# Kernel tuning notes

Hardware: AMD Instinct MI355X
Metric: run time of the kernel (lower is better)

The kernel has to match this reference:

```python
import jax, jax.numpy as jnp
import numpy as np

POOL = (2, 2)
STRIDES = (2, 2)


def _extract_patches(x, ph, pw, sh, sw):
    # x: [B, W, H, C] -> [B, Wo, Ho, ph*pw, C], patch elems ordered (di*pw + dj)
    B, W, H, C = x.shape
    Wo = (W - ph) // sh + 1
    Ho = (H - pw) // sw + 1
    slabs = [x[:, di:di + sh * (Wo - 1) + 1:sh, dj:dj + sw * (Ho - 1) + 1:sw, :]
             for di in range(ph) for dj in range(pw)]
    return jnp.stack(slabs, axis=3)


def setup_inputs() -> dict:
    key = jax.random.key(0)
    k1, _ = jax.random.split(key)
    inputs = jax.random.normal(k1, (32, 224, 224, 64), dtype=jnp.float32)
    mask = jnp.ones((1,), dtype=jnp.float32)  # learnable blend scalar
    return {"inputs": inputs, "mask": mask}


def reference(inputs, mask):
    ph, pw = POOL
    sh, sw = STRIDES
    patches = _extract_patches(inputs, ph, pw, sh, sw)  # [B,Wo,Ho,K,C]

    # exponential-maximum (softmax-weighted) pooling over window axis
    em_w = jax.nn.softmax(patches, axis=3)
    em_pool = jnp.sum(patches * em_w, axis=3)  # [B,Wo,Ho,C]

    # eDSCW pooling: Dice-Sorensen coefficient vs window mean, softmax-weighted
    x_avg = jnp.mean(patches, axis=3, keepdims=True)
    dsc = 2.0 * (x_avg * patches) / (x_avg * x_avg + patches * patches)
    dsc_w = jax.nn.softmax(dsc, axis=3)
    dsc_pool = jnp.sum(patches * dsc_w, axis=3)  # [B,Wo,Ho,C]

    return em_pool * mask + dsc_pool * (1.0 - mask)
```

## Files before the change

### kernel.cpp

```cpp
#include <hip/hip_runtime.h>


constexpr int Bn = 32;
constexpr int Wd = 224;
constexpr int Hd = 224;
constexpr int Cd = 64;
constexpr int Wo = 112;
constexpr int Ho = 112;
constexpr int HC = Hd * Cd;
constexpr int TOTAL4 = Bn * Wo * Ho * (Cd / 4);

__global__ __launch_bounds__(256)
void adapool2d_kernel(const float* __restrict__ in,
                      const float* __restrict__ mask,
                      float* __restrict__ out) {
    int i = blockIdx.x * 256 + threadIdx.x;
    if (i >= TOTAL4) return;

    const float m  = mask[0];
    const float m1 = 1.0f - m;

    int c4 = (i & 15) * 4;
    int t  = i >> 4;
    int ho = t % Ho;
    t      = t / Ho;
    int wo = t % Wo;
    int b  = t / Wo;

    const float* p = in + (size_t)(b * Wd + 2 * wo) * HC + (2 * ho) * Cd + c4;
    float4 v00 = *reinterpret_cast<const float4*>(p);
    float4 v01 = *reinterpret_cast<const float4*>(p + Cd);
    float4 v10 = *reinterpret_cast<const float4*>(p + HC);
    float4 v11 = *reinterpret_cast<const float4*>(p + HC + Cd);

    float q0[4] = {v00.x, v00.y, v00.z, v00.w};
    float q1[4] = {v01.x, v01.y, v01.z, v01.w};
    float q2[4] = {v10.x, v10.y, v10.z, v10.w};
    float q3[4] = {v11.x, v11.y, v11.z, v11.w};
    float r[4];

#pragma unroll
    for (int k = 0; k < 4; ++k) {
        float a  = q0[k], bb = q1[k], cc = q2[k], dd = q3[k];

        float ea = __expf(a), eb = __expf(bb), ec = __expf(cc), ed = __expf(dd);
        float inv_se = __builtin_amdgcn_rcpf(ea + eb + ec + ed);
        float em = (a * ea + bb * eb + cc * ec + dd * ed) * inv_se;

        float avg  = 0.25f * (a + bb + cc + dd);
        float avg2 = avg * avg;
        float ta   = 2.0f * avg;
        float da = ta * a  * __builtin_amdgcn_rcpf(avg2 + a  * a);
        float db = ta * bb * __builtin_amdgcn_rcpf(avg2 + bb * bb);
        float dc = ta * cc * __builtin_amdgcn_rcpf(avg2 + cc * cc);
        float de = ta * dd * __builtin_amdgcn_rcpf(avg2 + dd * dd);
        float fa = __expf(da), fb = __expf(db), fc = __expf(dc), fd = __expf(de);
        float inv_sd = __builtin_amdgcn_rcpf(fa + fb + fc + fd);
        float dp = (a * fa + bb * fb + cc * fc + dd * fd) * inv_sd;

        r[k] = em * m + dp * m1;
    }

    float4 o = make_float4(r[0], r[1], r[2], r[3]);
    reinterpret_cast<float4*>(out)[i] = o;
}

extern "C" void kernel_launch(void* const* d_in, const int* in_sizes, int n_in,
                              void* d_out, int out_size, void* d_ws, size_t ws_size,
                              hipStream_t stream) {
    const float* in   = (const float*)d_in[0];
    const float* mask = (const float*)d_in[1];
    float* out        = (float*)d_out;

    constexpr int threads = 256;
    constexpr int blocks  = (TOTAL4 + threads - 1) / threads;
    adapool2d_kernel<<<blocks, threads, 0, stream>>>(in, mask, out);
}
```

Before: 548.6 us.

## Load contiguous row segments per wave and pair windows via lane shuffles

Remaps threads so each wave reads a contiguous segment of the top and bottom input rows with one float4 load each, then exchanges horizontal neighbours via __shfl_xor instead of issuing separate loads. This aims to make global loads fully contiguous and halve per-lane load instructions. In exchange, twice as many threads are launched, each window's math is computed redundantly by two lanes, and half the lanes skip the store.

```diff
diff --git a/kernel.cpp b/kernel.cpp
--- a/kernel.cpp
+++ b/kernel.cpp
@@ -8,30 +8,42 @@
 constexpr int Wo = 112;
 constexpr int Ho = 112;
 constexpr int HC = Hd * Cd;
-constexpr int TOTAL4 = Bn * Wo * Ho * (Cd / 4);
+constexpr int WAVES_PER_WO = Hd / 4;
+constexpr int TOTAL_WAVES = Bn * Wo * WAVES_PER_WO;
+constexpr int BLOCKS = TOTAL_WAVES / 4;
 
 __global__ __launch_bounds__(256)
 void adapool2d_kernel(const float* __restrict__ in,
                       const float* __restrict__ mask,
                       float* __restrict__ out) {
-    int i = blockIdx.x * 256 + threadIdx.x;
-    if (i >= TOTAL4) return;
+    const int lane = threadIdx.x & 63;
+    const int wv   = (blockIdx.x << 2) | (threadIdx.x >> 6);
+
+    const int hblk = wv % WAVES_PER_WO;
+    int t          = wv / WAVES_PER_WO;
+    const int wo   = t % Wo;
+    const int b    = t / Wo;
+    const int h0   = hblk * 4;
 
     const float m  = mask[0];
     const float m1 = 1.0f - m;
 
-    int c4 = (i & 15) * 4;
-    int t  = i >> 4;
-    int ho = t % Ho;
-    t      = t / Ho;
-    int wo = t % Wo;
-    int b  = t / Wo;
+    const float* ptop = in + (size_t)(b * Wd + 2 * wo) * HC + h0 * Cd + lane * 4;
+    const float* pbot = ptop + HC;
+    float4 At = *reinterpret_cast<const float4*>(ptop);
+    float4 Bt = *reinterpret_cast<const float4*>(pbot);
 
-    const float* p = in + (size_t)(b * Wd + 2 * wo) * HC + (2 * ho) * Cd + c4;
-    float4 v00 = *reinterpret_cast<const float4*>(p);
-    float4 v01 = *reinterpret_cast<const float4*>(p + Cd);
-    float4 v10 = *reinterpret_cast<const float4*>(p + HC);
-    float4 v11 = *reinterpret_cast<const float4*>(p + HC + Cd);
+    float4 Ax, Bx;
+    Ax.x = __shfl_xor(At.x, 16); Ax.y = __shfl_xor(At.y, 16);
+    Ax.z = __shfl_xor(At.z, 16); Ax.w = __shfl_xor(At.w, 16);
+    Bx.x = __shfl_xor(Bt.x, 16); Bx.y = __shfl_xor(Bt.y, 16);
+    Bx.z = __shfl_xor(Bt.z, 16); Bx.w = __shfl_xor(Bt.w, 16);
+
+    const bool odd = (lane & 16) != 0;
+    float4 v00 = odd ? Ax : At;
+    float4 v01 = odd ? At : Ax;
+    float4 v10 = odd ? Bx : Bt;
+    float4 v11 = odd ? Bt : Bx;
 
     float q0[4] = {v00.x, v00.y, v00.z, v00.w};
     float q1[4] = {v01.x, v01.y, v01.z, v01.w};
@@ -61,8 +73,12 @@
         r[k] = em * m + dp * m1;
     }
 
-    float4 o = make_float4(r[0], r[1], r[2], r[3]);
-    reinterpret_cast<float4*>(out)[i] = o;
+    if (!odd) {
+        const int ho = (h0 >> 1) + ((lane >> 5) & 1);
+        const int c4 = lane & 15;
+        float4 o = make_float4(r[0], r[1], r[2], r[3]);
+        reinterpret_cast<float4*>(out)[(size_t)((b * Wo + wo) * Ho + ho) * 16 + c4] = o;
+    }
 }
 
 extern "C" void kernel_launch(void* const* d_in, const int* in_sizes, int n_in,
@@ -72,7 +88,5 @@
     const float* mask = (const float*)d_in[1];
     float* out        = (float*)d_out;
 
-    constexpr int threads = 256;
-    constexpr int blocks  = (TOTAL4 + threads - 1) / threads;
-    adapool2d_kernel<<<blocks, threads, 0, stream>>>(in, mask, out);
+    adapool2d_kernel<<<BLOCKS, 256, 0, stream>>>(in, mask, out);
 }
```

Result: no change. 555.8 us (+1.3%).
